# Kernel optimization log

Measured on AMD Instinct MI355X. Metric: run time of the kernel, lower is better.

Reference implementation:

```python
import jax, jax.numpy as jnp
import numpy as np
from jax.ops import segment_sum

HIDDEN = 128  # hard-coded in VGAEModel.__init__


def gcn_conv(x, W, b, src, dst, n_nodes):
    """PyG GCNConv: h = x@W; add self-loops; symmetric norm D^-1/2 A D^-1/2; scatter-add; +bias."""
    h = x @ W  # [N, out]
    loop = jnp.arange(n_nodes, dtype=src.dtype)
    s = jnp.concatenate([src, loop])  # [E+N]
    d = jnp.concatenate([dst, loop])  # [E+N]
    deg = segment_sum(jnp.ones_like(d, dtype=h.dtype), d, num_segments=n_nodes)  # [N]
    dinv = jnp.where(deg > 0, jax.lax.rsqrt(deg), 0.0)
    norm = dinv[s] * dinv[d]  # [E+N]
    msg = h[s] * norm[:, None]  # [E+N, out] -- largest intermediate
    out = segment_sum(msg, d, num_segments=n_nodes)  # [N, out]
    return out + b


def setup_inputs() -> dict:
    key = jax.random.key(0)
    ks = jax.random.split(key, 8)
    N, E, IN, OUT = 50000, 1600000, 256, 64
    x = jax.random.normal(ks[0], (N, IN), dtype=jnp.float32)
    edge_index = jax.random.randint(ks[1], (2, E), 0, N, dtype=jnp.int32)
    sc = lambda fan_in: 1.0 / np.sqrt(fan_in)
    W1 = jax.random.uniform(ks[2], (IN, HIDDEN), jnp.float32, -sc(IN), sc(IN))
    b1 = jnp.zeros((HIDDEN,), jnp.float32)
    W_mu = jax.random.uniform(ks[3], (HIDDEN, OUT), jnp.float32, -sc(HIDDEN), sc(HIDDEN))
    b_mu = jnp.zeros((OUT,), jnp.float32)
    W_ls = jax.random.uniform(ks[4], (HIDDEN, OUT), jnp.float32, -sc(HIDDEN), sc(HIDDEN))
    b_ls = jnp.zeros((OUT,), jnp.float32)
    return {"x": x, "edge_index": edge_index, "n_nodes": N,
            "W1": W1, "b1": b1, "W_mu": W_mu, "b_mu": b_mu, "W_ls": W_ls, "b_ls": b_ls}


def reference(x, edge_index, n_nodes, W1, b1, W_mu, b_mu, W_ls, b_ls):
    src, dst = edge_index[0], edge_index[1]
    h = jax.nn.relu(gcn_conv(x, W1, b1, src, dst, n_nodes))
    mu = gcn_conv(h, W_mu, b_mu, src, dst, n_nodes)
    logstd = gcn_conv(h, W_ls, b_ls, src, dst, n_nodes)
    return (mu, logstd)
```

## Files before the change

kernel.cpp:

```cpp
#include <hip/hip_runtime.h>
#include <hip/hip_fp16.h>


#define IN_DIM 256
#define F1 128
#define F2 64
#define BN 128
#define CAP 4736
#define BIN_EDGES 4096

typedef _Float16 f16x8 __attribute__((ext_vector_type(8)));
typedef float f32x4 __attribute__((ext_vector_type(4)));

static inline int cdiv_i(int a, int b) { return (a + b - 1) / b; }

__global__ void k_prep_frags(const float* __restrict__ W1,
                             const float* __restrict__ Wmu,
                             const float* __restrict__ Wls,
                             __half* __restrict__ W1frag,
                             __half* __restrict__ Wcfrag) {
    int t = blockIdx.x * blockDim.x + threadIdx.x;
    if (t < 8 * 8 * 64) {
        int lane = t & 63, nt = (t >> 6) & 7, ks = t >> 9;
        int k0 = ks * 32 + ((lane >> 4) << 3);
        int n = nt * 16 + (lane & 15);
#pragma unroll
        for (int j = 0; j < 8; ++j)
            W1frag[(size_t)t * 8 + j] = __float2half(W1[(k0 + j) * F1 + n]);
    } else if (t < 8 * 8 * 64 + 4 * 8 * 64) {
        int u = t - 8 * 8 * 64;
        int lane = u & 63, nt = (u >> 6) & 7, ks = u >> 9;
        int k0 = ks * 32 + ((lane >> 4) << 3);
        int c = nt * 16 + (lane & 15);
        const float* W = (c < F2) ? (Wmu + c) : (Wls + (c - F2));
#pragma unroll
        for (int j = 0; j < 8; ++j)
            Wcfrag[(size_t)u * 8 + j] = __float2half(W[(k0 + j) * F2]);
    }
}

__global__ __launch_bounds__(512) void k_binning(const int* __restrict__ src,
                                                 const int* __restrict__ dst,
                                                 int* __restrict__ bcur,
                                                 int* __restrict__ pairs, int E) {
    __shared__ int hcnt[512];
    __shared__ int hrank[512];
    __shared__ int hbase[512];
    __shared__ int lbase[512];
    __shared__ int stage[BIN_EDGES];
    __shared__ int gaddr[BIN_EDGES];
    const int tid = threadIdx.x;
    hcnt[tid] = 0; hrank[tid] = 0;
    __syncthreads();
    const int e0 = blockIdx.x * BIN_EDGES;
    int s_[8], d_[8];
#pragma unroll
    for (int it = 0; it < 8; ++it) {
        int e = e0 + it * 512 + tid;
        if (e < E) {
            s_[it] = src[e];
            d_[it] = dst[e];
            atomicAdd(&hcnt[d_[it] >> 7], 1);
        } else {
            d_[it] = -1;
        }
    }
    __syncthreads();
    int v = hcnt[tid];
    lbase[tid] = v;
    __syncthreads();
    for (int ofs = 1; ofs < 512; ofs <<= 1) {
        int add = (tid >= ofs) ? lbase[tid - ofs] : 0;
        __syncthreads();
        lbase[tid] += add;
        __syncthreads();
    }
    int total = lbase[511];
    int excl = lbase[tid] - v;
    __syncthreads();
    lbase[tid] = excl;
    hbase[tid] = v ? atomicAdd(&bcur[tid], v) : 0;
    __syncthreads();
#pragma unroll
    for (int it = 0; it < 8; ++it) {
        if (d_[it] >= 0) {
            int b = d_[it] >> 7;
            int r = atomicAdd(&hrank[b], 1);
            int li = lbase[b] + r;
            stage[li] = ((d_[it] & (BN - 1)) << 16) | s_[it];
            gaddr[li] = b * CAP + hbase[b] + r;
        }
    }
    __syncthreads();
    for (int i = tid; i < total; i += 512)
        pairs[gaddr[i]] = stage[i];
}

__global__ __launch_bounds__(512) void k_bucket_build(const int* __restrict__ pairs,
                                                      const int* __restrict__ bcur,
                                                      float* __restrict__ dinv,
                                                      int* __restrict__ rs,
                                                      int* __restrict__ re,
                                                      int* __restrict__ ssrc, int N) {
    __shared__ int hist[BN];
    __shared__ int offs[BN];
    __shared__ int stage[CAP];
    const int b = blockIdx.x;
    const int n0 = b * BN;
    const int tid = threadIdx.x;
    const int pbase = b * CAP;
    const int cnt = min(bcur[b], CAP);
    if (tid < BN) hist[tid] = 0;
    __syncthreads();
    for (int e = tid; e < cnt; e += 512)
        atomicAdd(&hist[pairs[pbase + e] >> 16], 1);
    __syncthreads();
    if (tid < BN) offs[tid] = hist[tid];
    __syncthreads();
    for (int ofs = 1; ofs < BN; ofs <<= 1) {
        int add = 0;
        if (tid < BN && tid >= ofs) add = offs[tid - ofs];
        __syncthreads();
        if (tid < BN) offs[tid] += add;
        __syncthreads();
    }
    if (tid < BN) {
        int incl = offs[tid];
        int excl = incl - hist[tid];
        int n = n0 + tid;
        if (n < N) {
            dinv[n] = rsqrtf((float)hist[tid] + 1.0f);
            rs[n] = pbase + excl;
            re[n] = pbase + incl;
        }
        offs[tid] = excl;
    }
    __syncthreads();
    for (int e = tid; e < cnt; e += 512) {
        int p = pairs[pbase + e];
        int idx = atomicAdd(&offs[p >> 16], 1);
        stage[idx] = p & 0xFFFF;
    }
    __syncthreads();
    for (int i = tid; i < cnt; i += 512) ssrc[pbase + i] = stage[i];
}

__global__ __launch_bounds__(256) void k_gemm1_mfma(const float* __restrict__ x,
                                                    const __half* __restrict__ W1frag,
                                                    __half* __restrict__ C, int M) {
    const int wave = threadIdx.x >> 6;
    const int lane = threadIdx.x & 63;
    const int m0 = blockIdx.x * 64 + wave * 16;
    if (m0 >= M) return;
    const int q = lane >> 4;
    const int arow = m0 + (lane & 15);
    f32x4 acc[8] = {};
#pragma unroll
    for (int ks = 0; ks < 8; ++ks) {
        const float* ap = x + (size_t)arow * IN_DIM + ks * 32 + q * 8;
        float4 f0 = *(const float4*)(ap);
        float4 f1 = *(const float4*)(ap + 4);
        f16x8 a = { (_Float16)f0.x, (_Float16)f0.y, (_Float16)f0.z, (_Float16)f0.w,
                    (_Float16)f1.x, (_Float16)f1.y, (_Float16)f1.z, (_Float16)f1.w };
        const __half* bbase = W1frag + ((size_t)(ks * 8) * 64 + lane) * 8;
#pragma unroll
        for (int nt = 0; nt < 8; ++nt) {
            f16x8 bfrag = *(const f16x8*)(bbase + (size_t)nt * 64 * 8);
            acc[nt] = __builtin_amdgcn_mfma_f32_16x16x32_f16(a, bfrag, acc[nt], 0, 0, 0);
        }
    }
#pragma unroll
    for (int nt = 0; nt < 8; ++nt)
#pragma unroll
        for (int r = 0; r < 4; ++r)
            C[(size_t)(m0 + q * 4 + r) * F1 + nt * 16 + (lane & 15)] =
                __float2half(acc[nt][r]);
}

__global__ __launch_bounds__(256) void k_gemm2_mfma(const __half* __restrict__ A,
                                                    const __half* __restrict__ Wcfrag,
                                                    __half* __restrict__ C, int M) {
    const int wave = threadIdx.x >> 6;
    const int lane = threadIdx.x & 63;
    const int m0 = blockIdx.x * 64 + wave * 16;
    if (m0 >= M) return;
    const int q = lane >> 4;
    const int arow = m0 + (lane & 15);
    f32x4 acc[8] = {};
#pragma unroll
    for (int ks = 0; ks < 4; ++ks) {
        f16x8 a = *(const f16x8*)(A + (size_t)arow * F1 + ks * 32 + q * 8);
        const __half* bbase = Wcfrag + ((size_t)(ks * 8) * 64 + lane) * 8;
#pragma unroll
        for (int nt = 0; nt < 8; ++nt) {
            f16x8 bfrag = *(const f16x8*)(bbase + (size_t)nt * 64 * 8);
            acc[nt] = __builtin_amdgcn_mfma_f32_16x16x32_f16(a, bfrag, acc[nt], 0, 0, 0);
        }
    }
#pragma unroll
    for (int nt = 0; nt < 8; ++nt)
#pragma unroll
        for (int r = 0; r < 4; ++r)
            C[(size_t)(m0 + q * 4 + r) * F1 + nt * 16 + (lane & 15)] =
                __float2half(acc[nt][r]);
}

__global__ __launch_bounds__(256) void k_gather1(const int* __restrict__ rs,
                                                 const int* __restrict__ re,
                                                 const int* __restrict__ ssrc,
                                                 const float* __restrict__ dinv,
                                                 const __half* __restrict__ t,
                                                 const float* __restrict__ b1,
                                                 __half* __restrict__ h, int N) {
    int node = (blockIdx.x * blockDim.x + threadIdx.x) >> 6;
    int lane = threadIdx.x & 63;
    if (node >= N) return;
    const int slot = lane >> 4;
    const int c16 = lane & 15;
    float di = dinv[node];
    float acc[8] = {};
    int e = rs[node] + slot, end = re[node];
    for (; e + 4 < end; e += 8) {
        int s0 = ssrc[e], s1 = ssrc[e + 4];
        float w0 = dinv[s0] * di, w1 = dinv[s1] * di;
        f16x8 v0 = *(const f16x8*)(t + (size_t)s0 * F1 + c16 * 8);
        f16x8 v1 = *(const f16x8*)(t + (size_t)s1 * F1 + c16 * 8);
#pragma unroll
        for (int j = 0; j < 8; ++j)
            acc[j] += (float)v0[j] * w0 + (float)v1[j] * w1;
    }
    if (e < end) {
        int s = ssrc[e];
        float w = dinv[s] * di;
        f16x8 v = *(const f16x8*)(t + (size_t)s * F1 + c16 * 8);
#pragma unroll
        for (int j = 0; j < 8; ++j) acc[j] += (float)v[j] * w;
    }
#pragma unroll
    for (int j = 0; j < 8; ++j) {
        acc[j] += __shfl_xor(acc[j], 16, 64);
        acc[j] += __shfl_xor(acc[j], 32, 64);
    }
    if (lane < 16) {
        f16x8 sv = *(const f16x8*)(t + (size_t)node * F1 + lane * 8);
        float4 bA = *(const float4*)(b1 + lane * 8);
        float4 bB = *(const float4*)(b1 + lane * 8 + 4);
        float bb[8] = { bA.x, bA.y, bA.z, bA.w, bB.x, bB.y, bB.z, bB.w };
        f16x8 o;
#pragma unroll
        for (int j = 0; j < 8; ++j) {
            float val = acc[j] + (float)sv[j] * di * di + bb[j];
            o[j] = (_Float16)fmaxf(val, 0.f);
        }
        *(f16x8*)(h + (size_t)node * F1 + lane * 8) = o;
    }
}

__global__ __launch_bounds__(256) void k_gather2(const int* __restrict__ rs,
                                                 const int* __restrict__ re,
                                                 const int* __restrict__ ssrc,
                                                 const float* __restrict__ dinv,
                                                 const __half* __restrict__ t,
                                                 const float* __restrict__ bmu,
                                                 const float* __restrict__ bls,
                                                 float* __restrict__ out, int N) {
    int node = (blockIdx.x * blockDim.x + threadIdx.x) >> 6;
    int lane = threadIdx.x & 63;
    if (node >= N) return;
    const int slot = lane >> 4;
    const int c16 = lane & 15;
    float di = dinv[node];
    float acc[8] = {};
    int e = rs[node] + slot, end = re[node];
    for (; e + 4 < end; e += 8) {
        int s0 = ssrc[e], s1 = ssrc[e + 4];
        float w0 = dinv[s0] * di, w1 = dinv[s1] * di;
        f16x8 v0 = *(const f16x8*)(t + (size_t)s0 * F1 + c16 * 8);
        f16x8 v1 = *(const f16x8*)(t + (size_t)s1 * F1 + c16 * 8);
#pragma unroll
        for (int j = 0; j < 8; ++j)
            acc[j] += (float)v0[j] * w0 + (float)v1[j] * w1;
    }
    if (e < end) {
        int s = ssrc[e];
        float w = dinv[s] * di;
        f16x8 v = *(const f16x8*)(t + (size_t)s * F1 + c16 * 8);
#pragma unroll
        for (int j = 0; j < 8; ++j) acc[j] += (float)v[j] * w;
    }
#pragma unroll
    for (int j = 0; j < 8; ++j) {
        acc[j] += __shfl_xor(acc[j], 16, 64);
        acc[j] += __shfl_xor(acc[j], 32, 64);
    }
    if (lane < 16) {
        f16x8 sv = *(const f16x8*)(t + (size_t)node * F1 + lane * 8);
        const float* bp = (lane < 8) ? (bmu + lane * 8) : (bls + lane * 8 - F2);
        float* op = (lane < 8) ? (out + (size_t)node * F2 + lane * 8)
                               : (out + (size_t)N * F2 + (size_t)node * F2 + lane * 8 - F2);
        float4 bA = *(const float4*)(bp);
        float4 bB = *(const float4*)(bp + 4);
        float bb[8] = { bA.x, bA.y, bA.z, bA.w, bB.x, bB.y, bB.z, bB.w };
        float4 oA, oB;
        oA.x = acc[0] + (float)sv[0] * di * di + bb[0];
        oA.y = acc[1] + (float)sv[1] * di * di + bb[1];
        oA.z = acc[2] + (float)sv[2] * di * di + bb[2];
        oA.w = acc[3] + (float)sv[3] * di * di + bb[3];
        oB.x = acc[4] + (float)sv[4] * di * di + bb[4];
        oB.y = acc[5] + (float)sv[5] * di * di + bb[5];
        oB.z = acc[6] + (float)sv[6] * di * di + bb[6];
        oB.w = acc[7] + (float)sv[7] * di * di + bb[7];
        *(float4*)(op) = oA;
        *(float4*)(op + 4) = oB;
    }
}

extern "C" void kernel_launch(void* const* d_in, const int* in_sizes, int n_in,
                              void* d_out, int out_size, void* d_ws, size_t ws_size,
                              hipStream_t stream) {
    const float* x   = (const float*)d_in[0];
    const int*   ei  = (const int*)d_in[1];
    const float* W1  = (const float*)d_in[3];
    const float* b1  = (const float*)d_in[4];
    const float* Wmu = (const float*)d_in[5];
    const float* bmu = (const float*)d_in[6];
    const float* Wls = (const float*)d_in[7];
    const float* bls = (const float*)d_in[8];

    const int N = in_sizes[0] / IN_DIM;
    const int E = in_sizes[1] / 2;
    const int* src = ei;
    const int* dst = ei + E;
    float* out = (float*)d_out;
    const int nbuck = cdiv_i(N, BN);

    size_t off = 0;
    auto carve = [&](size_t n) { size_t o = off; off += (n + 3) & ~(size_t)3; return o; };
    float* ws = (float*)d_ws;
    float*  dinv   =        ws + carve(N);
    int*    rs     = (int*)(ws + carve(N));
    int*    re     = (int*)(ws + carve(N));
    int*    bcur   = (int*)(ws + carve(512));
    int*    ssrc   = (int*)(ws + carve((size_t)nbuck * CAP));
    __half* t16    = (__half*)(ws + carve((size_t)N * F1 / 2));
    __half* h16    = (__half*)(ws + carve((size_t)N * F1 / 2));
    __half* W1frag = (__half*)(ws + carve(8 * 8 * 64 * 8 / 2));
    __half* Wcfrag = (__half*)(ws + carve(4 * 8 * 64 * 8 / 2));
    (void)ws_size;
    int* pairs = (int*)t16;
    __half* t2_16 = t16;

    k_prep_frags<<<cdiv_i(8 * 8 * 64 + 4 * 8 * 64, 256), 256, 0, stream>>>(
        W1, Wmu, Wls, W1frag, Wcfrag);

    hipMemsetAsync(bcur, 0, sizeof(int) * 512, stream);
    k_binning<<<cdiv_i(E, BIN_EDGES), 512, 0, stream>>>(src, dst, bcur, pairs, E);
    k_bucket_build<<<nbuck, 512, 0, stream>>>(pairs, bcur, dinv, rs, re, ssrc, N);

    k_gemm1_mfma<<<cdiv_i(N, 64), 256, 0, stream>>>(x, W1frag, t16, N);
    k_gather1<<<cdiv_i(N * 64, 256), 256, 0, stream>>>(rs, re, ssrc, dinv,
                                                       t16, b1, h16, N);
    k_gemm2_mfma<<<cdiv_i(N, 64), 256, 0, stream>>>(h16, Wcfrag, t2_16, N);
    k_gather2<<<cdiv_i(N * 64, 256), 256, 0, stream>>>(rs, re, ssrc, dinv,
                                                       t2_16, bmu, bls, out, N);
}
```

Before: 297.6 us.

## Split feature matrices into column quarters and pre-scale rows by dinv

GEMM outputs are now stored in four column-quarter planes of 32 halves and pre-multiplied by the source node's dinv. The gathers therefore become plain sums with one final scale. Each gather block works on a single quarter across all nodes, so the working set per pass is a quarter of the feature matrix (about 3.2MB), which is meant to improve cache hit rates on the random neighbour reads. In exchange it launches four times as many wave-per-node tasks, re-reads the edge lists four times, and issues 16-byte gathers per lane group.

```diff
diff --git a/kernel.cpp b/kernel.cpp
--- a/kernel.cpp
+++ b/kernel.cpp
@@ -5,6 +5,7 @@
 #define IN_DIM 256
 #define F1 128
 #define F2 64
+#define QF 32
 #define BN 128
 #define CAP 4736
 #define BIN_EDGES 4096
@@ -147,6 +148,7 @@
 
 __global__ __launch_bounds__(256) void k_gemm1_mfma(const float* __restrict__ x,
                                                     const __half* __restrict__ W1frag,
+                                                    const float* __restrict__ dinv,
                                                     __half* __restrict__ C, int M) {
     const int wave = threadIdx.x >> 6;
     const int lane = threadIdx.x & 63;
@@ -158,8 +160,8 @@
 #pragma unroll
     for (int ks = 0; ks < 8; ++ks) {
         const float* ap = x + (size_t)arow * IN_DIM + ks * 32 + q * 8;
-        float4 f0 = *(const float4*)(ap);
-        float4 f1 = *(const float4*)(ap + 4);
+        f32x4 f0 = *(const f32x4*)(ap);
+        f32x4 f1 = *(const f32x4*)(ap + 4);
         f16x8 a = { (_Float16)f0.x, (_Float16)f0.y, (_Float16)f0.z, (_Float16)f0.w,
                     (_Float16)f1.x, (_Float16)f1.y, (_Float16)f1.z, (_Float16)f1.w };
         const __half* bbase = W1frag + ((size_t)(ks * 8) * 64 + lane) * 8;
@@ -169,16 +171,22 @@
             acc[nt] = __builtin_amdgcn_mfma_f32_16x16x32_f16(a, bfrag, acc[nt], 0, 0, 0);
         }
     }
-#pragma unroll
-    for (int nt = 0; nt < 8; ++nt)
+    float dv[4];
+#pragma unroll
+    for (int r = 0; r < 4; ++r) dv[r] = dinv[m0 + q * 4 + r];
+#pragma unroll
+    for (int nt = 0; nt < 8; ++nt) {
+        int col = nt * 16 + (lane & 15);
+        __half* cq = C + (size_t)(col >> 5) * M * QF + (col & 31);
 #pragma unroll
         for (int r = 0; r < 4; ++r)
-            C[(size_t)(m0 + q * 4 + r) * F1 + nt * 16 + (lane & 15)] =
-                __float2half(acc[nt][r]);
+            cq[(size_t)(m0 + q * 4 + r) * QF] = __float2half(acc[nt][r] * dv[r]);
+    }
 }
 
 __global__ __launch_bounds__(256) void k_gemm2_mfma(const __half* __restrict__ A,
                                                     const __half* __restrict__ Wcfrag,
+                                                    const float* __restrict__ dinv,
                                                     __half* __restrict__ C, int M) {
     const int wave = threadIdx.x >> 6;
     const int lane = threadIdx.x & 63;
@@ -189,7 +197,7 @@
     f32x4 acc[8] = {};
 #pragma unroll
     for (int ks = 0; ks < 4; ++ks) {
-        f16x8 a = *(const f16x8*)(A + (size_t)arow * F1 + ks * 32 + q * 8);
+        f16x8 a = *(const f16x8*)(A + (size_t)ks * M * QF + (size_t)arow * QF + q * 8);
         const __half* bbase = Wcfrag + ((size_t)(ks * 8) * 64 + lane) * 8;
 #pragma unroll
         for (int nt = 0; nt < 8; ++nt) {
@@ -197,12 +205,17 @@
             acc[nt] = __builtin_amdgcn_mfma_f32_16x16x32_f16(a, bfrag, acc[nt], 0, 0, 0);
         }
     }
-#pragma unroll
-    for (int nt = 0; nt < 8; ++nt)
+    float dv[4];
+#pragma unroll
+    for (int r = 0; r < 4; ++r) dv[r] = dinv[m0 + q * 4 + r];
+#pragma unroll
+    for (int nt = 0; nt < 8; ++nt) {
+        int col = nt * 16 + (lane & 15);
+        __half* cq = C + (size_t)(col >> 5) * M * QF + (col & 31);
 #pragma unroll
         for (int r = 0; r < 4; ++r)
-            C[(size_t)(m0 + q * 4 + r) * F1 + nt * 16 + (lane & 15)] =
-                __float2half(acc[nt][r]);
+            cq[(size_t)(m0 + q * 4 + r) * QF] = __float2half(acc[nt][r] * dv[r]);
+    }
 }
 
 __global__ __launch_bounds__(256) void k_gather1(const int* __restrict__ rs,
@@ -211,48 +224,54 @@
                                                  const float* __restrict__ dinv,
                                                  const __half* __restrict__ t,
                                                  const float* __restrict__ b1,
-                                                 __half* __restrict__ h, int N) {
-    int node = (blockIdx.x * blockDim.x + threadIdx.x) >> 6;
-    int lane = threadIdx.x & 63;
+                                                 __half* __restrict__ h,
+                                                 int N, int NBW) {
+    const int wave = threadIdx.x >> 6;
+    const int lane = threadIdx.x & 63;
+    const int q = blockIdx.x / NBW;
+    const int node = (blockIdx.x - q * NBW) * 4 + wave;
     if (node >= N) return;
-    const int slot = lane >> 4;
-    const int c16 = lane & 15;
-    float di = dinv[node];
+    const int slot = lane >> 2;
+    const int c4 = lane & 3;
+    const __half* tq = t + (size_t)q * N * QF;
     float acc[8] = {};
     int e = rs[node] + slot, end = re[node];
-    for (; e + 4 < end; e += 8) {
-        int s0 = ssrc[e], s1 = ssrc[e + 4];
-        float w0 = dinv[s0] * di, w1 = dinv[s1] * di;
-        f16x8 v0 = *(const f16x8*)(t + (size_t)s0 * F1 + c16 * 8);
-        f16x8 v1 = *(const f16x8*)(t + (size_t)s1 * F1 + c16 * 8);
-#pragma unroll
-        for (int j = 0; j < 8; ++j)
-            acc[j] += (float)v0[j] * w0 + (float)v1[j] * w1;
+    for (; e + 16 < end; e += 32) {
+        int s0 = ssrc[e], s1 = ssrc[e + 16];
+        f16x8 v0 = *(const f16x8*)(tq + (size_t)s0 * QF + c4 * 8);
+        f16x8 v1 = *(const f16x8*)(tq + (size_t)s1 * QF + c4 * 8);
+#pragma unroll
+        for (int j = 0; j < 8; ++j)
+            acc[j] += (float)v0[j] + (float)v1[j];
     }
     if (e < end) {
         int s = ssrc[e];
-        float w = dinv[s] * di;
-        f16x8 v = *(const f16x8*)(t + (size_t)s * F1 + c16 * 8);
-#pragma unroll
-        for (int j = 0; j < 8; ++j) acc[j] += (float)v[j] * w;
+        f16x8 v = *(const f16x8*)(tq + (size_t)s * QF + c4 * 8);
+#pragma unroll
+        for (int j = 0; j < 8; ++j) acc[j] += (float)v[j];
     }
 #pragma unroll
     for (int j = 0; j < 8; ++j) {
+        acc[j] += __shfl_xor(acc[j], 4, 64);
+        acc[j] += __shfl_xor(acc[j], 8, 64);
         acc[j] += __shfl_xor(acc[j], 16, 64);
         acc[j] += __shfl_xor(acc[j], 32, 64);
     }
-    if (lane < 16) {
-        f16x8 sv = *(const f16x8*)(t + (size_t)node * F1 + lane * 8);
-        float4 bA = *(const float4*)(b1 + lane * 8);
-        float4 bB = *(const float4*)(b1 + lane * 8 + 4);
+    if (lane < 4) {
+        float di = dinv[node];
+        f16x8 sv = *(const f16x8*)(tq + (size_t)node * QF + lane * 8);
+        const float* bp = b1 + q * QF + lane * 8;
+        f32x4 bA = *(const f32x4*)(bp);
+        f32x4 bB = *(const f32x4*)(bp + 4);
         float bb[8] = { bA.x, bA.y, bA.z, bA.w, bB.x, bB.y, bB.z, bB.w };
         f16x8 o;
 #pragma unroll
         for (int j = 0; j < 8; ++j) {
-            float val = acc[j] + (float)sv[j] * di * di + bb[j];
+            float val = (acc[j] + (float)sv[j]) * di + bb[j];
             o[j] = (_Float16)fmaxf(val, 0.f);
         }
-        *(f16x8*)(h + (size_t)node * F1 + lane * 8) = o;
+        __builtin_nontemporal_store(
+            o, (f16x8*)(h + (size_t)q * N * QF + (size_t)node * QF + lane * 8));
     }
 }
 
@@ -263,55 +282,58 @@
                                                  const __half* __restrict__ t,
                                                  const float* __restrict__ bmu,
                                                  const float* __restrict__ bls,
-                                                 float* __restrict__ out, int N) {
-    int node = (blockIdx.x * blockDim.x + threadIdx.x) >> 6;
-    int lane = threadIdx.x & 63;
+                                                 float* __restrict__ out,
+                                                 int N, int NBW) {
+    const int wave = threadIdx.x >> 6;
+    const int lane = threadIdx.x & 63;
+    const int q = blockIdx.x / NBW;
+    const int node = (blockIdx.x - q * NBW) * 4 + wave;
     if (node >= N) return;
-    const int slot = lane >> 4;
-    const int c16 = lane & 15;
-    float di = dinv[node];
+    const int slot = lane >> 2;
+    const int c4 = lane & 3;
+    const __half* tq = t + (size_t)q * N * QF;
     float acc[8] = {};
     int e = rs[node] + slot, end = re[node];
-    for (; e + 4 < end; e += 8) {
-        int s0 = ssrc[e], s1 = ssrc[e + 4];
-        float w0 = dinv[s0] * di, w1 = dinv[s1] * di;
-        f16x8 v0 = *(const f16x8*)(t + (size_t)s0 * F1 + c16 * 8);
-        f16x8 v1 = *(const f16x8*)(t + (size_t)s1 * F1 + c16 * 8);
-#pragma unroll
-        for (int j = 0; j < 8; ++j)
-            acc[j] += (float)v0[j] * w0 + (float)v1[j] * w1;
+    for (; e + 16 < end; e += 32) {
+        int s0 = ssrc[e], s1 = ssrc[e + 16];
+        f16x8 v0 = *(const f16x8*)(tq + (size_t)s0 * QF + c4 * 8);
+        f16x8 v1 = *(const f16x8*)(tq + (size_t)s1 * QF + c4 * 8);
+#pragma unroll
+        for (int j = 0; j < 8; ++j)
+            acc[j] += (float)v0[j] + (float)v1[j];
     }
     if (e < end) {
         int s = ssrc[e];
-        float w = dinv[s] * di;
-        f16x8 v = *(const f16x8*)(t + (size_t)s * F1 + c16 * 8);
-#pragma unroll
-        for (int j = 0; j < 8; ++j) acc[j] += (float)v[j] * w;
+        f16x8 v = *(const f16x8*)(tq + (size_t)s * QF + c4 * 8);
+#pragma unroll
+        for (int j = 0; j < 8; ++j) acc[j] += (float)v[j];
     }
 #pragma unroll
     for (int j = 0; j < 8; ++j) {
+        acc[j] += __shfl_xor(acc[j], 4, 64);
+        acc[j] += __shfl_xor(acc[j], 8, 64);
         acc[j] += __shfl_xor(acc[j], 16, 64);
         acc[j] += __shfl_xor(acc[j], 32, 64);
     }
-    if (lane < 16) {
-        f16x8 sv = *(const f16x8*)(t + (size_t)node * F1 + lane * 8);
-        const float* bp = (lane < 8) ? (bmu + lane * 8) : (bls + lane * 8 - F2);
-        float* op = (lane < 8) ? (out + (size_t)node * F2 + lane * 8)
-                               : (out + (size_t)N * F2 + (size_t)node * F2 + lane * 8 - F2);
-        float4 bA = *(const float4*)(bp);
-        float4 bB = *(const float4*)(bp + 4);
+    if (lane < 4) {
+        float di = dinv[node];
+        f16x8 sv = *(const f16x8*)(tq + (size_t)node * QF + lane * 8);
+        const float* bp = (q < 2) ? (bmu + q * QF + lane * 8)
+                                  : (bls + (q - 2) * QF + lane * 8);
+        float* op = (q < 2)
+            ? (out + (size_t)node * F2 + q * QF + lane * 8)
+            : (out + (size_t)N * F2 + (size_t)node * F2 + (q - 2) * QF + lane * 8);
+        f32x4 bA = *(const f32x4*)(bp);
+        f32x4 bB = *(const f32x4*)(bp + 4);
         float bb[8] = { bA.x, bA.y, bA.z, bA.w, bB.x, bB.y, bB.z, bB.w };
-        float4 oA, oB;
-        oA.x = acc[0] + (float)sv[0] * di * di + bb[0];
-        oA.y = acc[1] + (float)sv[1] * di * di + bb[1];
-        oA.z = acc[2] + (float)sv[2] * di * di + bb[2];
-        oA.w = acc[3] + (float)sv[3] * di * di + bb[3];
-        oB.x = acc[4] + (float)sv[4] * di * di + bb[4];
-        oB.y = acc[5] + (float)sv[5] * di * di + bb[5];
-        oB.z = acc[6] + (float)sv[6] * di * di + bb[6];
-        oB.w = acc[7] + (float)sv[7] * di * di + bb[7];
-        *(float4*)(op) = oA;
-        *(float4*)(op + 4) = oB;
+        float r[8];
+#pragma unroll
+        for (int j = 0; j < 8; ++j)
+            r[j] = (acc[j] + (float)sv[j]) * di + bb[j];
+        f32x4 oA = { r[0], r[1], r[2], r[3] };
+        f32x4 oB = { r[4], r[5], r[6], r[7] };
+        __builtin_nontemporal_store(oA, (f32x4*)(op));
+        __builtin_nontemporal_store(oB, (f32x4*)(op + 4));
     }
 }
 
@@ -357,10 +379,11 @@
     k_binning<<<cdiv_i(E, BIN_EDGES), 512, 0, stream>>>(src, dst, bcur, pairs, E);
     k_bucket_build<<<nbuck, 512, 0, stream>>>(pairs, bcur, dinv, rs, re, ssrc, N);
 
-    k_gemm1_mfma<<<cdiv_i(N, 64), 256, 0, stream>>>(x, W1frag, t16, N);
-    k_gather1<<<cdiv_i(N * 64, 256), 256, 0, stream>>>(rs, re, ssrc, dinv,
-                                                       t16, b1, h16, N);
-    k_gemm2_mfma<<<cdiv_i(N, 64), 256, 0, stream>>>(h16, Wcfrag, t2_16, N);
-    k_gather2<<<cdiv_i(N * 64, 256), 256, 0, stream>>>(rs, re, ssrc, dinv,
-                                                       t2_16, bmu, bls, out, N);
-}
+    const int NBW = cdiv_i(N, 4);
+
+    k_gemm1_mfma<<<cdiv_i(N, 64), 256, 0, stream>>>(x, W1frag, dinv, t16, N);
+    k_gather1<<<4 * NBW, 256, 0, stream>>>(rs, re, ssrc, dinv, t16, b1, h16, N, NBW);
+    k_gemm2_mfma<<<cdiv_i(N, 64), 256, 0, stream>>>(h16, Wcfrag, dinv, t2_16, N);
+    k_gather2<<<4 * NBW, 256, 0, stream>>>(rs, re, ssrc, dinv, t2_16, bmu, bls,
+                                           out, N, NBW);
+}
```

Result: slower. 325.4 us (+9.3%).
